# Kernel optimization log

Hardware: AMD Instinct MI355X
Metric: run time of the kernel (lower is better)

## Reference

```python
import jax, jax.numpy as jnp
import numpy as np

C = 256
B, H, W = 16, 48, 48


def setup_inputs() -> dict:
    key = jax.random.key(0)
    ks = jax.random.split(key, 9)
    s = 1.0 / np.sqrt(C)
    return {
        "x": jax.random.normal(ks[0], (B, C, H, W), dtype=jnp.float32),
        "Wq": jax.random.normal(ks[1], (C, C), dtype=jnp.float32) * s,
        "bq": jax.random.normal(ks[2], (C,), dtype=jnp.float32) * s,
        "Wk": jax.random.normal(ks[3], (C, C), dtype=jnp.float32) * s,
        "bk": jax.random.normal(ks[4], (C,), dtype=jnp.float32) * s,
        "Wv": jax.random.normal(ks[5], (C, C), dtype=jnp.float32) * s,
        "bv": jax.random.normal(ks[6], (C,), dtype=jnp.float32) * s,
        "rel_h": jax.random.normal(ks[7], (1, C, 1, H), dtype=jnp.float32),
        "rel_w": jax.random.normal(ks[8], (1, C, W, 1), dtype=jnp.float32),
    }


def reference(x, Wq, bq, Wk, bk, Wv, bv, rel_h, rel_w):
    b, c, h, w = x.shape
    n = h * w
    # 1x1 conv == per-pixel linear over channels
    def proj(Wp, bp):
        y = jnp.einsum('bchw,oc->bohw', x, Wp) + bp[None, :, None, None]
        return y.reshape(b, c, n)
    q = proj(Wq, bq)  # [B, C, N]
    k = proj(Wk, bk)
    v = proj(Wv, bv)
    # content-content: q^T k -> [B, N, N]
    cc = jnp.einsum('bcn,bcm->bnm', q, k)
    # relative position term: (rel_h + rel_w) -> [1, C, W, H] -> [C, N]
    pos = (rel_h + rel_w).reshape(c, n)
    # content-position: pos^T @ q -> [B, N, N]
    cp = jnp.einsum('cn,bcm->bnm', pos, q)
    att = jax.nn.softmax(cc + cp, axis=-1)  # [B, N, N]
    # out[b,c,n] = sum_m v[b,c,m] * att[b,n,m]
    out = jnp.einsum('bcm,bnm->bcn', v, att)
    return out.reshape(b, c, h, w)
```

## Files before the change

### kernel.cpp

```cpp
#include <hip/hip_runtime.h>
#include <hip/hip_bf16.h>


#define BB 16
#define CC 256
#define HH 48
#define NN 2304

typedef float f32x4 __attribute__((ext_vector_type(4)));
typedef short bf16x8 __attribute__((ext_vector_type(8)));
typedef _Float16 f16x8 __attribute__((ext_vector_type(8)));

#define MFMA(a, b, c)  __builtin_amdgcn_mfma_f32_16x16x32_bf16((a), (b), (c), 0, 0, 0)
#define MFMAH(a, b, c) __builtin_amdgcn_mfma_f32_16x16x32_f16((a), (b), (c), 0, 0, 0)

__device__ inline bf16x8 ldg8(const __hip_bfloat16* p) {
    return *reinterpret_cast<const bf16x8*>(p);
}
__device__ inline f16x8 ldh8(const _Float16* p) {
    return *reinterpret_cast<const f16x8*>(p);
}
__device__ inline float bf2f(unsigned short v) {
    unsigned u = (unsigned)v << 16;
    float f;
    __builtin_memcpy(&f, &u, 4);
    return f;
}

typedef __attribute__((address_space(3))) unsigned int lds_uint;
typedef const __attribute__((address_space(1))) unsigned int gbl_uint;

__device__ inline void gload_lds16(const void* g, void* l) {
    __builtin_amdgcn_global_load_lds((gbl_uint*)g, (lds_uint*)l, 16, 0, 0);
}

__global__ __launch_bounds__(256) void k_prep_x(const float* __restrict__ x,
        _Float16* __restrict__ xt_hi, _Float16* __restrict__ xt_lo) {
    __shared__ float tile[64][65];
    int b = blockIdx.z, n0 = blockIdx.x * 64, c0 = blockIdx.y * 64;
    const float* xb = x + (size_t)b * CC * NN;
    #pragma unroll
    for (int i = 0; i < 16; ++i) {
        int idx = i * 256 + threadIdx.x;
        int r = idx >> 6, col = idx & 63;
        tile[r][col] = xb[(size_t)(c0 + r) * NN + n0 + col];
    }
    __syncthreads();
    #pragma unroll
    for (int i = 0; i < 16; ++i) {
        int idx = i * 256 + threadIdx.x;
        int r = idx >> 6, col = idx & 63;
        float v = tile[col][r];
        _Float16 h = (_Float16)v;
        size_t o = ((size_t)b * NN + n0 + r) * CC + c0 + col;
        xt_hi[o] = h;
        xt_lo[o] = (_Float16)(v - (float)h);
    }
}

__global__ __launch_bounds__(256) void k_prep_w(const float* __restrict__ Wq,
        const float* __restrict__ Wk, const float* __restrict__ Wv,
        _Float16* __restrict__ w) {
    int i = blockIdx.x * 256 + threadIdx.x;
    int m = i >> 16, j = i & 65535;
    const float* W = (m == 0) ? Wq : ((m == 1) ? Wk : Wv);
    w[i] = (_Float16)W[j];
}

__global__ __launch_bounds__(256) void k_prep_rel(const float* __restrict__ rel_h,
        const float* __restrict__ rel_w,
        _Float16* __restrict__ relhT, _Float16* __restrict__ relwT) {
    int i = blockIdx.x * 256 + threadIdx.x;
    int h = i >> 8, c = i & 255;
    relhT[i] = (_Float16)rel_h[c * HH + h];
    relwT[i] = (_Float16)rel_w[c * HH + h];
}

__global__ __launch_bounds__(256) void k_proj(
        const _Float16* __restrict__ xt_hi, const _Float16* __restrict__ xt_lo,
        const _Float16* __restrict__ w,
        const float* __restrict__ bq, const float* __restrict__ bk, const float* __restrict__ bv,
        _Float16* __restrict__ qt_hi, _Float16* __restrict__ qt_lo,
        _Float16* __restrict__ kt,
        __hip_bfloat16* __restrict__ vbuf) {
    __shared__ __align__(16) _Float16 lds_a[2][32][256];
    int b = blockIdx.y, pj = blockIdx.z;
    int n0 = blockIdx.x * 32;
    int wave = threadIdx.x >> 6, lane = threadIdx.x & 63;
    int lr = lane & 15, lg = lane >> 4;
    int o0 = wave * 64;
    const size_t bN = (size_t)b * NN;
    const _Float16* wp = w + (size_t)pj * 65536;

    {
        int r_in = lane >> 5, chunk = lane & 31;
        #pragma unroll
        for (int j = 0; j < 4; ++j) {
            int lrow = wave * 8 + 2 * j;
            int row = lrow + r_in;
            gload_lds16(xt_hi + (bN + n0 + row) * CC + ((chunk ^ (row & 7)) * 8),
                        &lds_a[0][lrow][0]);
            gload_lds16(xt_lo + (bN + n0 + row) * CC + ((chunk ^ (row & 7)) * 8),
                        &lds_a[1][lrow][0]);
        }
    }
    __syncthreads();

    f32x4 acc[2][4] = {};
    #pragma unroll
    for (int ks = 0; ks < 8; ++ks) {
        int kk = ks * 32 + lg * 8;
        f16x8 ah[2], al[2];
        #pragma unroll
        for (int nt = 0; nt < 2; ++nt) {
            int row = nt * 16 + lr;
            int ch = ((ks * 4 + lg) ^ (lr & 7)) * 8;
            ah[nt] = *reinterpret_cast<const f16x8*>(&lds_a[0][row][ch]);
            al[nt] = *reinterpret_cast<const f16x8*>(&lds_a[1][row][ch]);
        }
        #pragma unroll
        for (int ot = 0; ot < 4; ++ot) {
            int rowB = o0 + ot * 16 + lr;
            f16x8 bh = ldh8(wp + rowB * CC + kk);
            #pragma unroll
            for (int nt = 0; nt < 2; ++nt) {
                acc[nt][ot] = MFMAH(ah[nt], bh, acc[nt][ot]);
                if (pj < 2) acc[nt][ot] = MFMAH(al[nt], bh, acc[nt][ot]);
            }
        }
    }
    const float* bias = (pj == 0) ? bq : ((pj == 1) ? bk : bv);
    #pragma unroll
    for (int ot = 0; ot < 4; ++ot) {
        int o = o0 + ot * 16 + lr;
        float bb = bias[o];
        #pragma unroll
        for (int nt = 0; nt < 2; ++nt) {
            #pragma unroll
            for (int r = 0; r < 4; ++r) {
                int n = n0 + nt * 16 + lg * 4 + r;
                float y = acc[nt][ot][r] + bb;
                if (pj == 0) {
                    _Float16 h = (_Float16)y;
                    size_t off = (bN + n) * CC + o;
                    qt_hi[off] = h;
                    qt_lo[off] = (_Float16)(y - (float)h);
                } else if (pj == 1) {
                    kt[(bN + n) * CC + o] = (_Float16)y;
                } else {
                    vbuf[((size_t)b * CC + o) * NN + n] = __float2bfloat16(y);
                }
            }
        }
    }
}

__global__ __launch_bounds__(256) void k_posq(
        const _Float16* __restrict__ qt_hi, const _Float16* __restrict__ qt_lo,
        const _Float16* __restrict__ relhT, const _Float16* __restrict__ relwT,
        float* __restrict__ rhq, float* __restrict__ rwq) {
    int b = blockIdx.y, m0 = blockIdx.x * 64;
    int wave = threadIdx.x >> 6, lane = threadIdx.x & 63;
    int lr = lane & 15, lg = lane >> 4;
    int m = m0 + wave * 16 + lr;
    const size_t bN = (size_t)b * NN;
    f32x4 acc[6] = {};
    #pragma unroll
    for (int ks = 0; ks < 8; ++ks) {
        int kk = ks * 32 + lg * 8;
        f16x8 bhf = ldh8(qt_hi + (bN + m) * CC + kk);
        f16x8 blf = ldh8(qt_lo + (bN + m) * CC + kk);
        #pragma unroll
        for (int t = 0; t < 3; ++t) {
            int rowH = t * 16 + lr;
            f16x8 ahh = ldh8(relhT + rowH * CC + kk);
            acc[t] = MFMAH(ahh, bhf, acc[t]);
            acc[t] = MFMAH(ahh, blf, acc[t]);
            f16x8 awh = ldh8(relwT + rowH * CC + kk);
            acc[3 + t] = MFMAH(awh, bhf, acc[3 + t]);
            acc[3 + t] = MFMAH(awh, blf, acc[3 + t]);
        }
    }
    #pragma unroll
    for (int t = 0; t < 3; ++t) {
        #pragma unroll
        for (int r = 0; r < 4; ++r) {
            int h = t * 16 + lg * 4 + r;
            rhq[((size_t)b * HH + h) * NN + m] = acc[t][r];
            rwq[((size_t)b * HH + h) * NN + m] = acc[3 + t][r];
        }
    }
}

__global__ __launch_bounds__(512, 2) void k_attn(
        const _Float16* __restrict__ qt_hi,
        const _Float16* __restrict__ kt,
        const float* __restrict__ rhq, const float* __restrict__ rwq,
        const __hip_bfloat16* __restrict__ vbuf,
        __hip_bfloat16* __restrict__ o0, __hip_bfloat16* __restrict__ o1,
        __hip_bfloat16* __restrict__ o2, __hip_bfloat16* __restrict__ o3,
        float2* __restrict__ ml, int tpb) {
    __shared__ __align__(16) _Float16 lds_k[2][64][128];
    __shared__ __align__(16) __hip_bfloat16 lds_v[256][64];
    __shared__ __align__(16) __hip_bfloat16 lds_p[128][64];
    float* lds_scale = reinterpret_cast<float*>(&lds_k[1][0][0]);
    int*   lds_flag  = reinterpret_cast<int*>(lds_scale + 128);
    int b = blockIdx.y;
    int n0 = blockIdx.x * 128;
    int z = blockIdx.z;
    int t0 = z * tpb, t_end = t0 + tpb;
    __hip_bfloat16* opart = (z == 0) ? o0 : (z == 1) ? o1 : (z == 2) ? o2 : o3;
    int wave = threadIdx.x >> 6, lane = threadIdx.x & 63;
    int lr = lane & 15, lg = lane >> 4;
    int rowA = n0 + wave * 16 + lr;
    const size_t bN = (size_t)b * NN;

    f16x8 qh[8];
    #pragma unroll
    for (int ks = 0; ks < 8; ++ks) {
        int kk = ks * 32 + lg * 8;
        qh[ks] = ldh8(qt_hi + (bN + rowA) * CC + kk);
    }
    int hn[4], wn[4];
    #pragma unroll
    for (int r = 0; r < 4; ++r) {
        int n = n0 + wave * 16 + lg * 4 + r;
        hn[r] = n % HH;
        wn[r] = n / HH;
    }
    const float* rhq_b = rhq + (size_t)b * HH * NN;
    const float* rwq_b = rwq + (size_t)b * HH * NN;

    int nh = wave >> 2;
    int cq = wave & 3;
    f32x4 oacc[4][4] = {};
    float mrun[4] = {-1e30f, -1e30f, -1e30f, -1e30f};
    float lrun[4] = {0.f, 0.f, 0.f, 0.f};

    int krin = lane >> 4, kch = lane & 15;
    auto STAGE_K = [&](int buf, int m0s, int k0) {
        #pragma unroll
        for (int j = 0; j < 2; ++j) {
            int lrow = wave * 8 + j * 4;
            int grow = lrow + krin;
            gload_lds16(kt + (bN + m0s + grow) * CC + k0 + ((kch ^ (grow & 7)) * 8),
                        &lds_k[buf][lrow][0]);
        }
    };
    int srl = lane >> 3;
    int sch = ((lane & 7) ^ srl) * 8;
    auto STAGE_V = [&](int half, int m0s) {
        #pragma unroll
        for (int j = 0; j < 2; ++j) {
            int lrow = half * 128 + wave * 16 + j * 8;
            int crow = lrow + srl;
            gload_lds16(vbuf + ((size_t)b * CC + crow) * NN + m0s + sch, &lds_v[lrow][0]);
        }
    };

    STAGE_K(0, t0 * 64, 0);
    __syncthreads();

    for (int t = t0; t < t_end; ++t) {
        int m0 = t * 64;
        float padd[4][4];
        #pragma unroll
        for (int mt = 0; mt < 4; ++mt) {
            int m = m0 + mt * 16 + lr;
            #pragma unroll
            for (int r = 0; r < 4; ++r)
                padd[mt][r] = rhq_b[(size_t)hn[r] * NN + m] + rwq_b[(size_t)wn[r] * NN + m];
        }
        f32x4 sacc[4] = {};
        #pragma unroll
        for (int s = 0; s < 2; ++s) {
            if (s == 0) {
                STAGE_K(1, m0, 128);
                STAGE_V(0, m0);
            } else {
                int mn = (t + 1 < t_end) ? (t + 1) * 64 : t0 * 64;
                STAGE_K(0, mn, 0);
                STAGE_V(1, m0);
            }
            #pragma unroll
            for (int ks = 0; ks < 4; ++ks) {
                #pragma unroll
                for (int mt = 0; mt < 4; ++mt) {
                    int row = mt * 16 + lr;
                    int ch = ((ks * 4 + lg) ^ (lr & 7)) * 8;
                    f16x8 bh = *reinterpret_cast<const f16x8*>(&lds_k[s][row][ch]);
                    sacc[mt] = MFMAH(qh[s * 4 + ks], bh, sacc[mt]);
                }
            }
            __syncthreads();
        }
        #pragma unroll
        for (int mt = 0; mt < 4; ++mt)
            #pragma unroll
            for (int r = 0; r < 4; ++r)
                sacc[mt][r] += padd[mt][r];
        bool lane_need = false;
        #pragma unroll
        for (int mt = 0; mt < 4; ++mt)
            #pragma unroll
            for (int r = 0; r < 4; ++r)
                lane_need |= (sacc[mt][r] > mrun[r] + 8.0f);
        bool wave_need = __any(lane_need);
        float scl_r[4] = {1.f, 1.f, 1.f, 1.f};
        if (wave_need) {
            #pragma unroll
            for (int r = 0; r < 4; ++r) {
                float smax = fmaxf(fmaxf(sacc[0][r], sacc[1][r]),
                                   fmaxf(sacc[2][r], sacc[3][r]));
                #pragma unroll
                for (int mk = 1; mk <= 8; mk <<= 1)
                    smax = fmaxf(smax, __shfl_xor(smax, mk));
                float mnew = fmaxf(mrun[r], smax);
                scl_r[r] = __expf(mrun[r] - mnew);
                mrun[r] = mnew;
                lrun[r] *= scl_r[r];
            }
        }
        #pragma unroll
        for (int r = 0; r < 4; ++r) {
            float rsum = 0.f;
            #pragma unroll
            for (int mt = 0; mt < 4; ++mt) {
                float p = __expf(sacc[mt][r] - mrun[r]);
                sacc[mt][r] = p;
                rsum += p;
            }
            lrun[r] += rsum;
        }
        #pragma unroll
        for (int mt = 0; mt < 4; ++mt) {
            #pragma unroll
            for (int r = 0; r < 4; ++r) {
                int prow = wave * 16 + lg * 4 + r;
                int pcol = mt * 16 + lr;
                int pcol_s = (((pcol >> 3) ^ (prow & 7)) << 3) | (pcol & 7);
                lds_p[prow][pcol_s] = __float2bfloat16(sacc[mt][r]);
            }
        }
        if (lr == 0) {
            #pragma unroll
            for (int r = 0; r < 4; ++r)
                lds_scale[wave * 16 + lg * 4 + r] = scl_r[r];
        }
        if (lane == 0) lds_flag[wave] = wave_need ? 1 : 0;
        __syncthreads();
        int4 f0 = *reinterpret_cast<const int4*>(&lds_flag[0]);
        int4 f1 = *reinterpret_cast<const int4*>(&lds_flag[4]);
        bool do_scale = (f0.x | f0.y | f0.z | f0.w | f1.x | f1.y | f1.z | f1.w) != 0;
        if (do_scale) {
            #pragma unroll
            for (int nf = 0; nf < 4; ++nf) {
                f32x4 s4 = *reinterpret_cast<const f32x4*>(&lds_scale[nh * 64 + nf * 16 + lg * 4]);
                #pragma unroll
                for (int cf = 0; cf < 4; ++cf)
                    oacc[nf][cf] *= s4;
            }
        }
        #pragma unroll
        for (int ks2 = 0; ks2 < 2; ++ks2) {
            bf16x8 pa[4];
            #pragma unroll
            for (int nf = 0; nf < 4; ++nf) {
                int prow = nh * 64 + nf * 16 + lr;
                int pch = ((ks2 * 4 + lg) ^ (lr & 7)) * 8;
                pa[nf] = *reinterpret_cast<const bf16x8*>(&lds_p[prow][pch]);
            }
            #pragma unroll
            for (int cf = 0; cf < 4; ++cf) {
                int vrow = cq * 64 + cf * 16 + lr;
                int vch = ((ks2 * 4 + lg) ^ (lr & 7)) * 8;
                bf16x8 bv = *reinterpret_cast<const bf16x8*>(&lds_v[vrow][vch]);
                #pragma unroll
                for (int nf = 0; nf < 4; ++nf)
                    oacc[nf][cf] = MFMA(pa[nf], bv, oacc[nf][cf]);
            }
        }
        __syncthreads();
    }
    #pragma unroll
    for (int r = 0; r < 4; ++r) {
        #pragma unroll
        for (int mk = 1; mk <= 8; mk <<= 1)
            lrun[r] += __shfl_xor(lrun[r], mk);
    }
    if (lr == 0) {
        #pragma unroll
        for (int r = 0; r < 4; ++r) {
            int n = n0 + wave * 16 + lg * 4 + r;
            ml[((size_t)z * BB + b) * NN + n] = make_float2(mrun[r], lrun[r]);
        }
    }
    #pragma unroll
    for (int nf = 0; nf < 4; ++nf) {
        int nbase = n0 + nh * 64 + nf * 16 + lg * 4;
        #pragma unroll
        for (int cf = 0; cf < 4; ++cf) {
            int c = cq * 64 + cf * 16 + lr;
            union { ushort4 u4; unsigned short us[4]; } pk;
            #pragma unroll
            for (int j = 0; j < 4; ++j) {
                __hip_bfloat16 hv = __float2bfloat16(oacc[nf][cf][j]);
                pk.us[j] = *reinterpret_cast<unsigned short*>(&hv);
            }
            *reinterpret_cast<ushort4*>(&opart[((size_t)b * CC + c) * NN + nbase]) = pk.u4;
        }
    }
}

__global__ __launch_bounds__(256) void k_combine(
        const __hip_bfloat16* __restrict__ o0, const __hip_bfloat16* __restrict__ o1,
        const __hip_bfloat16* __restrict__ o2, const __hip_bfloat16* __restrict__ o3,
        const float2* __restrict__ ml, int nsplit, float* __restrict__ out) {
    size_t idx = ((size_t)blockIdx.x * 256 + threadIdx.x) * 4;
    int n4 = (int)(idx % NN);
    int c  = (int)((idx / NN) % CC);
    int b  = (int)(idx / ((size_t)NN * CC));
    float M[4] = {-1e30f, -1e30f, -1e30f, -1e30f};
    for (int zz = 0; zz < nsplit; ++zz) {
        #pragma unroll
        for (int j = 0; j < 4; ++j)
            M[j] = fmaxf(M[j], ml[((size_t)zz * BB + b) * NN + n4 + j].x);
    }
    float num[4] = {}, den[4] = {};
    for (int zz = 0; zz < nsplit; ++zz) {
        const __hip_bfloat16* op = (zz == 0) ? o0 : (zz == 1) ? o1 : (zz == 2) ? o2 : o3;
        ushort4 u = *reinterpret_cast<const ushort4*>(op + ((size_t)b * CC + c) * NN + n4);
        unsigned short us[4] = {u.x, u.y, u.z, u.w};
        #pragma unroll
        for (int j = 0; j < 4; ++j) {
            float2 v = ml[((size_t)zz * BB + b) * NN + n4 + j];
            float w = __expf(v.x - M[j]);
            num[j] += bf2f(us[j]) * w;
            den[j] += v.y * w;
        }
    }
    f32x4 o;
    #pragma unroll
    for (int j = 0; j < 4; ++j) o[j] = num[j] / den[j];
    *reinterpret_cast<f32x4*>(&out[idx]) = o;
}

extern "C" void kernel_launch(void* const* d_in, const int* in_sizes, int n_in,
                              void* d_out, int out_size, void* d_ws, size_t ws_size,
                              hipStream_t stream) {
    const float* x     = (const float*)d_in[0];
    const float* Wq    = (const float*)d_in[1];
    const float* bq    = (const float*)d_in[2];
    const float* Wk    = (const float*)d_in[3];
    const float* bk    = (const float*)d_in[4];
    const float* Wv    = (const float*)d_in[5];
    const float* bv    = (const float*)d_in[6];
    const float* rel_h = (const float*)d_in[7];
    const float* rel_w = (const float*)d_in[8];
    float* out = (float*)d_out;

    size_t off = 0;
    auto carve = [&](size_t bytes) {
        void* p = (char*)d_ws + off;
        off += (bytes + 255) & ~(size_t)255;
        return p;
    };
    const size_t sz_t = (size_t)BB * NN * CC * 2;
    _Float16* xt_hi  = (_Float16*)carve(sz_t);
    _Float16* xt_lo  = (_Float16*)carve(sz_t);
    _Float16* qt_hi  = (_Float16*)carve(sz_t);
    _Float16* qt_lo  = (_Float16*)carve(sz_t);
    _Float16* kt     = (_Float16*)carve(sz_t);
    __hip_bfloat16* vbuf = (__hip_bfloat16*)carve(sz_t);
    _Float16* relhT = (_Float16*)carve((size_t)HH * CC * 2);
    _Float16* relwT = (_Float16*)carve((size_t)HH * CC * 2);
    _Float16* w     = (_Float16*)carve((size_t)3 * CC * CC * 2);
    float* rhq = (float*)carve((size_t)BB * HH * NN * 4);
    float* rwq = (float*)carve((size_t)BB * HH * NN * 4);
    float2* ml = (float2*)carve((size_t)4 * BB * NN * sizeof(float2));
    if (off > ws_size) return;

    __hip_bfloat16* o0 = (__hip_bfloat16*)xt_hi;
    __hip_bfloat16* o1 = (__hip_bfloat16*)xt_lo;
    __hip_bfloat16* o2 = nullptr;
    __hip_bfloat16* o3 = nullptr;
    int nsplit = 2;
    {
        size_t save = off;
        __hip_bfloat16* p2 = (__hip_bfloat16*)carve(sz_t);
        __hip_bfloat16* p3 = (__hip_bfloat16*)carve(sz_t);
        if (off <= ws_size) { nsplit = 4; o2 = p2; o3 = p3; }
        else { off = save; }
    }
    int tpb = 36 / nsplit;

    k_prep_x<<<dim3(NN / 64, CC / 64, BB), 256, 0, stream>>>(x, xt_hi, xt_lo);
    k_prep_w<<<dim3(3 * CC * CC / 256), 256, 0, stream>>>(Wq, Wk, Wv, w);
    k_prep_rel<<<dim3(HH * CC / 256), 256, 0, stream>>>(rel_h, rel_w, relhT, relwT);
    k_proj<<<dim3(NN / 32, BB, 3), 256, 0, stream>>>(
        xt_hi, xt_lo, w, bq, bk, bv, qt_hi, qt_lo, kt, vbuf);
    k_posq<<<dim3(NN / 64, BB), 256, 0, stream>>>(
        qt_hi, qt_lo, relhT, relwT, rhq, rwq);
    k_attn<<<dim3(NN / 128, BB, nsplit), 512, 0, stream>>>(
        qt_hi, kt, rhq, rwq, vbuf, o0, o1, o2, o3, ml, tpb);
    k_combine<<<dim3((size_t)BB * CC * NN / 1024), 256, 0, stream>>>(
        o0, o1, o2, o3, ml, nsplit, out);
}
```

Before: 455.9 us.

## Fuse x transpose/split into projection kernel and compute Q,K,V per block

Drops the separate x prep kernel and its fp16 hi/lo transposed buffers. The projection kernel now reads fp32 x directly, transposes it through LDS, splits it into hi/lo fp16 in LDS, and loops over all three projections inside one block, so x is read once instead of three times. This trades workspace traffic and a kernel launch for extra LDS use (about 65 KB per block), which may lower occupancy, and the grid now has a third as many blocks. The attention partial-output buffers are now carved separately instead of reusing the old x buffers.

```diff
diff --git a/kernel.cpp b/kernel.cpp
--- a/kernel.cpp
+++ b/kernel.cpp
@@ -32,30 +32,6 @@
 
 __device__ inline void gload_lds16(const void* g, void* l) {
     __builtin_amdgcn_global_load_lds((gbl_uint*)g, (lds_uint*)l, 16, 0, 0);
-}
-
-__global__ __launch_bounds__(256) void k_prep_x(const float* __restrict__ x,
-        _Float16* __restrict__ xt_hi, _Float16* __restrict__ xt_lo) {
-    __shared__ float tile[64][65];
-    int b = blockIdx.z, n0 = blockIdx.x * 64, c0 = blockIdx.y * 64;
-    const float* xb = x + (size_t)b * CC * NN;
-    #pragma unroll
-    for (int i = 0; i < 16; ++i) {
-        int idx = i * 256 + threadIdx.x;
-        int r = idx >> 6, col = idx & 63;
-        tile[r][col] = xb[(size_t)(c0 + r) * NN + n0 + col];
-    }
-    __syncthreads();
-    #pragma unroll
-    for (int i = 0; i < 16; ++i) {
-        int idx = i * 256 + threadIdx.x;
-        int r = idx >> 6, col = idx & 63;
-        float v = tile[col][r];
-        _Float16 h = (_Float16)v;
-        size_t o = ((size_t)b * NN + n0 + r) * CC + c0 + col;
-        xt_hi[o] = h;
-        xt_lo[o] = (_Float16)(v - (float)h);
-    }
 }
 
 __global__ __launch_bounds__(256) void k_prep_w(const float* __restrict__ Wq,
@@ -76,79 +52,93 @@
     relwT[i] = (_Float16)rel_w[c * HH + h];
 }
 
-__global__ __launch_bounds__(256) void k_proj(
-        const _Float16* __restrict__ xt_hi, const _Float16* __restrict__ xt_lo,
+__global__ __launch_bounds__(256) void k_projqkv(
+        const float* __restrict__ x,
         const _Float16* __restrict__ w,
         const float* __restrict__ bq, const float* __restrict__ bk, const float* __restrict__ bv,
         _Float16* __restrict__ qt_hi, _Float16* __restrict__ qt_lo,
         _Float16* __restrict__ kt,
         __hip_bfloat16* __restrict__ vbuf) {
+    __shared__ float xf[32][257];
     __shared__ __align__(16) _Float16 lds_a[2][32][256];
-    int b = blockIdx.y, pj = blockIdx.z;
+    int b = blockIdx.y;
     int n0 = blockIdx.x * 32;
-    int wave = threadIdx.x >> 6, lane = threadIdx.x & 63;
+    int t = threadIdx.x;
+    int wave = t >> 6, lane = t & 63;
     int lr = lane & 15, lg = lane >> 4;
     int o0 = wave * 64;
     const size_t bN = (size_t)b * NN;
-    const _Float16* wp = w + (size_t)pj * 65536;
 
     {
-        int r_in = lane >> 5, chunk = lane & 31;
-        #pragma unroll
-        for (int j = 0; j < 4; ++j) {
-            int lrow = wave * 8 + 2 * j;
-            int row = lrow + r_in;
-            gload_lds16(xt_hi + (bN + n0 + row) * CC + ((chunk ^ (row & 7)) * 8),
-                        &lds_a[0][lrow][0]);
-            gload_lds16(xt_lo + (bN + n0 + row) * CC + ((chunk ^ (row & 7)) * 8),
-                        &lds_a[1][lrow][0]);
+        int nj = t & 31, cg = t >> 5;
+        #pragma unroll
+        for (int it = 0; it < 32; ++it) {
+            int c = it * 8 + cg;
+            xf[nj][c] = x[((size_t)b * CC + c) * NN + n0 + nj];
         }
     }
     __syncthreads();
-
-    f32x4 acc[2][4] = {};
-    #pragma unroll
-    for (int ks = 0; ks < 8; ++ks) {
-        int kk = ks * 32 + lg * 8;
-        f16x8 ah[2], al[2];
-        #pragma unroll
-        for (int nt = 0; nt < 2; ++nt) {
-            int row = nt * 16 + lr;
-            int ch = ((ks * 4 + lg) ^ (lr & 7)) * 8;
-            ah[nt] = *reinterpret_cast<const f16x8*>(&lds_a[0][row][ch]);
-            al[nt] = *reinterpret_cast<const f16x8*>(&lds_a[1][row][ch]);
-        }
+    {
+        int r = t & 31, cg = t >> 5;
+        #pragma unroll
+        for (int i = 0; i < 32; ++i) {
+            int c = cg + 8 * i;
+            float v = xf[r][c];
+            _Float16 h = (_Float16)v;
+            int pc = (((c >> 3) ^ (r & 7)) << 3) | (c & 7);
+            lds_a[0][r][pc] = h;
+            lds_a[1][r][pc] = (_Float16)(v - (float)h);
+        }
+    }
+    __syncthreads();
+
+    #pragma unroll
+    for (int pj = 0; pj < 3; ++pj) {
+        const _Float16* wp = w + (size_t)pj * 65536;
+        f32x4 acc[2][4] = {};
+        #pragma unroll
+        for (int ks = 0; ks < 8; ++ks) {
+            int kk = ks * 32 + lg * 8;
+            f16x8 ah[2], al[2];
+            #pragma unroll
+            for (int nt = 0; nt < 2; ++nt) {
+                int row = nt * 16 + lr;
+                int ch = ((ks * 4 + lg) ^ (lr & 7)) * 8;
+                ah[nt] = *reinterpret_cast<const f16x8*>(&lds_a[0][row][ch]);
+                al[nt] = *reinterpret_cast<const f16x8*>(&lds_a[1][row][ch]);
+            }
+            #pragma unroll
+            for (int ot = 0; ot < 4; ++ot) {
+                int rowB = o0 + ot * 16 + lr;
+                f16x8 bh = ldh8(wp + rowB * CC + kk);
+                #pragma unroll
+                for (int nt = 0; nt < 2; ++nt) {
+                    acc[nt][ot] = MFMAH(ah[nt], bh, acc[nt][ot]);
+                    if (pj < 2) acc[nt][ot] = MFMAH(al[nt], bh, acc[nt][ot]);
+                }
+            }
+        }
+        const float* bias = (pj == 0) ? bq : ((pj == 1) ? bk : bv);
         #pragma unroll
         for (int ot = 0; ot < 4; ++ot) {
-            int rowB = o0 + ot * 16 + lr;
-            f16x8 bh = ldh8(wp + rowB * CC + kk);
+            int o = o0 + ot * 16 + lr;
+            float bb = bias[o];
             #pragma unroll
             for (int nt = 0; nt < 2; ++nt) {
-                acc[nt][ot] = MFMAH(ah[nt], bh, acc[nt][ot]);
-                if (pj < 2) acc[nt][ot] = MFMAH(al[nt], bh, acc[nt][ot]);
-            }
-        }
-    }
-    const float* bias = (pj == 0) ? bq : ((pj == 1) ? bk : bv);
-    #pragma unroll
-    for (int ot = 0; ot < 4; ++ot) {
-        int o = o0 + ot * 16 + lr;
-        float bb = bias[o];
-        #pragma unroll
-        for (int nt = 0; nt < 2; ++nt) {
-            #pragma unroll
-            for (int r = 0; r < 4; ++r) {
-                int n = n0 + nt * 16 + lg * 4 + r;
-                float y = acc[nt][ot][r] + bb;
-                if (pj == 0) {
-                    _Float16 h = (_Float16)y;
-                    size_t off = (bN + n) * CC + o;
-                    qt_hi[off] = h;
-                    qt_lo[off] = (_Float16)(y - (float)h);
-                } else if (pj == 1) {
-                    kt[(bN + n) * CC + o] = (_Float16)y;
-                } else {
-                    vbuf[((size_t)b * CC + o) * NN + n] = __float2bfloat16(y);
+                #pragma unroll
+                for (int r = 0; r < 4; ++r) {
+                    int n = n0 + nt * 16 + lg * 4 + r;
+                    float y = acc[nt][ot][r] + bb;
+                    if (pj == 0) {
+                        _Float16 h = (_Float16)y;
+                        size_t off = (bN + n) * CC + o;
+                        qt_hi[off] = h;
+                        qt_lo[off] = (_Float16)(y - (float)h);
+                    } else if (pj == 1) {
+                        kt[(bN + n) * CC + o] = (_Float16)y;
+                    } else {
+                        vbuf[((size_t)b * CC + o) * NN + n] = __float2bfloat16(y);
+                    }
                 }
             }
         }
@@ -466,8 +456,6 @@
         return p;
     };
     const size_t sz_t = (size_t)BB * NN * CC * 2;
-    _Float16* xt_hi  = (_Float16*)carve(sz_t);
-    _Float16* xt_lo  = (_Float16*)carve(sz_t);
     _Float16* qt_hi  = (_Float16*)carve(sz_t);
     _Float16* qt_lo  = (_Float16*)carve(sz_t);
     _Float16* kt     = (_Float16*)carve(sz_t);
@@ -478,10 +466,10 @@
     float* rhq = (float*)carve((size_t)BB * HH * NN * 4);
     float* rwq = (float*)carve((size_t)BB * HH * NN * 4);
     float2* ml = (float2*)carve((size_t)4 * BB * NN * sizeof(float2));
+    __hip_bfloat16* o0 = (__hip_bfloat16*)carve(sz_t);
+    __hip_bfloat16* o1 = (__hip_bfloat16*)carve(sz_t);
     if (off > ws_size) return;
 
-    __hip_bfloat16* o0 = (__hip_bfloat16*)xt_hi;
-    __hip_bfloat16* o1 = (__hip_bfloat16*)xt_lo;
     __hip_bfloat16* o2 = nullptr;
     __hip_bfloat16* o3 = nullptr;
     int nsplit = 2;
@@ -494,11 +482,10 @@
     }
     int tpb = 36 / nsplit;
 
-    k_prep_x<<<dim3(NN / 64, CC / 64, BB), 256, 0, stream>>>(x, xt_hi, xt_lo);
     k_prep_w<<<dim3(3 * CC * CC / 256), 256, 0, stream>>>(Wq, Wk, Wv, w);
     k_prep_rel<<<dim3(HH * CC / 256), 256, 0, stream>>>(rel_h, rel_w, relhT, relwT);
-    k_proj<<<dim3(NN / 32, BB, 3), 256, 0, stream>>>(
-        xt_hi, xt_lo, w, bq, bk, bv, qt_hi, qt_lo, kt, vbuf);
+    k_projqkv<<<dim3(NN / 32, BB), 256, 0, stream>>>(
+        x, w, bq, bk, bv, qt_hi, qt_lo, kt, vbuf);
     k_posq<<<dim3(NN / 64, BB), 256, 0, stream>>>(
         qt_hi, qt_lo, relhT, relwT, rhq, rwq);
     k_attn<<<dim3(NN / 128, BB, nsplit), 512, 0, stream>>>(
```

Measured after the change: 444.8 us. 2.4% less time.
